# Optimization experiments

Hardware: AMD Instinct MI355X
Metric: run time of the kernel (lower is better)

## Reference

```python
import jax, jax.numpy as jnp
import numpy as np

# Dims: B batch, L seq, D model dim, A attn dim, H heads, W window, FF ff hidden
B, L, D = 4, 4096, 1024
A, H, W = 64, 1, 64
FF = 2 * D
EPS = 1e-6


def setup_inputs() -> dict:
    key = jax.random.key(0)
    ks = jax.random.split(key, 12)
    s = lambda k, shape, scale: (jax.random.normal(k, shape, jnp.float32) * scale)
    return {
        "x": s(ks[0], (B, L, D), 1.0),
        "norm1_w": jnp.ones((D,), jnp.float32),
        "norm2_w": jnp.ones((D,), jnp.float32),
        "a_raw": s(ks[1], (D,), 1.0),   # diag SSM transition (pre-sigmoid)
        "b_w": s(ks[2], (D,), 0.5),     # diag input gain
        "c_w": s(ks[3], (D,), 0.5),     # diag output gain
        "Wq": s(ks[4], (D, A), D ** -0.5),
        "Wk": s(ks[5], (D, A), D ** -0.5),
        "Wv": s(ks[6], (D, A), D ** -0.5),
        "Wo": s(ks[7], (A, D), A ** -0.5),
        "Wg": s(ks[8], (D, 1), D ** -0.5),
        "gate_bias": jnp.float32(-4.0),
        "ff_w1": s(ks[9], (D, FF), D ** -0.5),
        "ff_w2": s(ks[10], (FF, D), FF ** -0.5),
    }


def rmsnorm(x, w):
    return x * jax.lax.rsqrt(jnp.mean(x * x, -1, keepdims=True) + EPS) * w


def ssm_scan(u, a):
    # h_t = a * h_{t-1} + u_t (diagonal linear recurrence), parallel assoc scan over time
    aa = jnp.broadcast_to(a, u.shape)

    def comb(c1, c2):
        a1, b1 = c1
        a2, b2 = c2
        return a1 * a2, a2 * b1 + b2

    _, h = jax.lax.associative_scan(comb, (aa, u), axis=1)
    return h


def reference(x, norm1_w, norm2_w, a_raw, b_w, c_w, Wq, Wk, Wv, Wo, Wg, gate_bias, ff_w1, ff_w2):
    normed = rmsnorm(x, norm1_w)                      # input_norm
    a = jax.nn.sigmoid(a_raw)                         # decay in (0,1)
    h = ssm_scan(normed * b_w, a)                     # ChaosSSMCore diag scan
    x_ssm = x + h * c_w                               # residual

    # Causal sliding-window attention sidecar (window W, includes self)
    K = x_ssm @ Wk                                    # [B,L,A]
    V = x_ssm @ Wv
    hd = A // H
    q = (x_ssm @ Wq).reshape(B, L, H, hd)
    idx = jnp.arange(L)[:, None] + jnp.arange(W)[None, :] - (W - 1)  # [L,W]
    valid = idx >= 0
    idxc = jnp.clip(idx, 0, L - 1)
    Kg = K[:, idxc].reshape(B, L, W, H, hd)           # gathered window keys
    Vg = V[:, idxc].reshape(B, L, W, H, hd)
    scores = jnp.einsum('blhd,blwhd->blhw', q, Kg) / jnp.sqrt(jnp.float32(hd))
    scores = jnp.where(valid[None, :, None, :], scores, -jnp.inf)
    p = jax.nn.softmax(scores, axis=-1)
    attn = jnp.einsum('blhw,blwhd->blhd', p, Vg).reshape(B, L, A) @ Wo

    gate = jax.nn.sigmoid(x_ssm @ Wg + gate_bias)     # near-zero gate at init
    x_ssm = x_ssm + gate * attn

    n2 = rmsnorm(x_ssm, norm2_w)                      # ff_norm
    y = x_ssm + jax.nn.silu(n2 @ ff_w1) @ ff_w2       # FeedForward residual
    return y
```

## Files before the change

kernel.cpp:

```cpp
#include <hip/hip_runtime.h>
#include <math.h>

#define B_ 4
#define L_ 4096
#define D_ 1024
#define A_ 64
#define FF_ 2048
#define N_ (B_*L_)
#define EPS_ 1e-6f
#define CHUNK_ 128
#define NCHUNK_ (L_/CHUNK_)

typedef __attribute__((ext_vector_type(8))) short bf16x8;
typedef __attribute__((ext_vector_type(4))) short s16x4;
typedef __attribute__((ext_vector_type(4))) float f32x4;

static __device__ __forceinline__ float sigmoidf_(float x) { return 1.f/(1.f+expf(-x)); }
static __device__ __forceinline__ float siluf_(float x)    { return x/(1.f+expf(-x)); }

static __device__ __forceinline__ unsigned short f2bf(float f) {
    unsigned u = __float_as_uint(f);
    u += 0x7fffu + ((u >> 16) & 1u);
    return (unsigned short)(u >> 16);
}

static __device__ __forceinline__ void gload16(const short* g, short* l) {
    __builtin_amdgcn_global_load_lds(
        (const __attribute__((address_space(1))) void*)g,
        (__attribute__((address_space(3))) void*)l, 16, 0, 0);
}

__global__ __launch_bounds__(256) void rms_kernel(const float* __restrict__ x,
                                                  float* __restrict__ rms)
{
    int row  = blockIdx.x*4 + (threadIdx.x>>6);
    int lane = threadIdx.x & 63;
    const float4* xr = (const float4*)(x + (size_t)row*D_);
    float s = 0.f;
#pragma unroll
    for (int j = 0; j < 4; j++) {
        float4 v = xr[lane + 64*j];
        s += v.x*v.x + v.y*v.y + v.z*v.z + v.w*v.w;
    }
#pragma unroll
    for (int off = 32; off > 0; off >>= 1) s += __shfl_xor(s, off);
    if (lane == 0) rms[row] = rsqrtf(s*(1.f/(float)D_) + EPS_);
}

__global__ __launch_bounds__(64) void scan1_kernel(
    const float* __restrict__ x, const float* __restrict__ rms1,
    const float* __restrict__ n1w, const float* __restrict__ bw,
    const float* __restrict__ araw, float* __restrict__ cpart)
{
    int d = blockIdx.x*64 + threadIdx.x;
    int c = blockIdx.y;
    int b = blockIdx.z;
    float a = sigmoidf_(araw[d]);
    float w = n1w[d]*bw[d];
    float h = 0.f;
    size_t base = ((size_t)b*L_ + (size_t)c*CHUNK_)*D_ + d;
    const float* rp = rms1 + b*L_ + c*CHUNK_;
#pragma unroll 8
    for (int t = 0; t < CHUNK_; t++) {
        float u = x[base + (size_t)t*D_] * rp[t] * w;
        h = a*h + u;
    }
    cpart[((size_t)b*NCHUNK_ + c)*D_ + d] = h;
}

__global__ __launch_bounds__(256) void scan2_kernel(
    const float* __restrict__ araw, const float* __restrict__ cpart,
    float* __restrict__ cin)
{
    int idx = blockIdx.x*256 + threadIdx.x;
    int b = idx >> 10;
    int d = idx & (D_-1);
    float a = sigmoidf_(araw[d]);
    float aT = a;
#pragma unroll
    for (int i = 0; i < 7; i++) aT *= aT;
    float cy = 0.f;
    for (int c = 0; c < NCHUNK_; c++) {
        size_t o = ((size_t)b*NCHUNK_ + c)*D_ + d;
        cin[o] = cy;
        cy = aT*cy + cpart[o];
    }
}

__global__ __launch_bounds__(64) void scan3_kernel(
    const float* __restrict__ x, const float* __restrict__ rms1,
    const float* __restrict__ n1w, const float* __restrict__ bw,
    const float* __restrict__ cw, const float* __restrict__ araw,
    const float* __restrict__ cin, float* __restrict__ x_ssm,
    short* __restrict__ xsb)
{
    int d = blockIdx.x*64 + threadIdx.x;
    int c = blockIdx.y;
    int b = blockIdx.z;
    float a = sigmoidf_(araw[d]);
    float w = n1w[d]*bw[d];
    float cwd = cw[d];
    float h = cin[((size_t)b*NCHUNK_ + c)*D_ + d];
    size_t base = ((size_t)b*L_ + (size_t)c*CHUNK_)*D_ + d;
    const float* rp = rms1 + b*L_ + c*CHUNK_;
#pragma unroll 8
    for (int t = 0; t < CHUNK_; t++) {
        size_t p = base + (size_t)t*D_;
        float xv = x[p];
        h = a*h + xv * rp[t] * w;
        float o = xv + h*cwd;
        x_ssm[p] = o;
        xsb[p] = (short)f2bf(o);
    }
}

__global__ __launch_bounds__(256) void gate_kernel(
    const float* __restrict__ xs, const float* __restrict__ Wg,
    const float* __restrict__ gb, float* __restrict__ gate)
{
    int row  = blockIdx.x*4 + (threadIdx.x>>6);
    int lane = threadIdx.x & 63;
    const float4* xr = (const float4*)(xs + (size_t)row*D_);
    const float4* wr = (const float4*)Wg;
    float s = 0.f;
#pragma unroll
    for (int j = 0; j < 4; j++) {
        float4 xv = xr[lane + 64*j];
        float4 wv = wr[lane + 64*j];
        s += xv.x*wv.x + xv.y*wv.y + xv.z*wv.z + xv.w*wv.w;
    }
#pragma unroll
    for (int off = 32; off > 0; off >>= 1) s += __shfl_xor(s, off);
    if (lane == 0) gate[row] = sigmoidf_(s + gb[0]);
}

__global__ __launch_bounds__(256) void attn_kernel(
    const float* __restrict__ qm, const float* __restrict__ km,
    const float* __restrict__ vm, short* __restrict__ om)
{
    __shared__ float KV[128][68];
    int b  = blockIdx.y;
    int l0 = blockIdx.x*64;
    int t  = threadIdx.x;
    int r  = t >> 2;
    int qq = t & 3;

#pragma unroll
    for (int i = 0; i < 8; i++) {
        int lin = i*256 + t;
        int row = lin >> 4;
        int f4  = lin & 15;
        int gl  = l0 - 64 + row;
        float4 val = make_float4(0.f,0.f,0.f,0.f);
        if (gl >= 0) val = *(const float4*)(km + ((size_t)b*L_ + gl)*A_ + f4*4);
        *(float4*)&KV[row][f4*4] = val;
    }
    float4 qreg[16];
    {
        const float* qrow = qm + ((size_t)b*L_ + l0 + r)*A_;
#pragma unroll
        for (int j = 0; j < 16; j++) qreg[j] = *(const float4*)(qrow + j*4);
    }
    __syncthreads();

    float s[16];
#pragma unroll
    for (int wi = 0; wi < 16; wi++) {
        int w  = qq*16 + wi;
        int tr = r + w + 1;
        float dot = 0.f;
#pragma unroll
        for (int j = 0; j < 16; j++) {
            float4 kv = *(const float4*)&KV[tr][j*4];
            dot += qreg[j].x*kv.x + qreg[j].y*kv.y + qreg[j].z*kv.z + qreg[j].w*kv.w;
        }
        s[wi] = (l0 + r - 63 + w >= 0) ? dot*0.125f : -INFINITY;
    }
    float mx = s[0];
#pragma unroll
    for (int wi = 1; wi < 16; wi++) mx = fmaxf(mx, s[wi]);
    mx = fmaxf(mx, __shfl_xor(mx, 1));
    mx = fmaxf(mx, __shfl_xor(mx, 2));
    float sum = 0.f;
#pragma unroll
    for (int wi = 0; wi < 16; wi++) { s[wi] = expf(s[wi] - mx); sum += s[wi]; }
    sum += __shfl_xor(sum, 1);
    sum += __shfl_xor(sum, 2);
    float inv = 1.f/sum;
#pragma unroll
    for (int wi = 0; wi < 16; wi++) s[wi] *= inv;

    __syncthreads();
#pragma unroll
    for (int i = 0; i < 8; i++) {
        int lin = i*256 + t;
        int row = lin >> 4;
        int f4  = lin & 15;
        int gl  = l0 - 64 + row;
        float4 val = make_float4(0.f,0.f,0.f,0.f);
        if (gl >= 0) val = *(const float4*)(vm + ((size_t)b*L_ + gl)*A_ + f4*4);
        *(float4*)&KV[row][f4*4] = val;
    }
    __syncthreads();

    float4 acc[4];
#pragma unroll
    for (int ss = 0; ss < 4; ss++) acc[ss] = make_float4(0.f,0.f,0.f,0.f);
#pragma unroll
    for (int w = 0; w < 64; w++) {
        float pv = __shfl(s[w & 15], (t & 60) + (w >> 4));
        int tr = r + w + 1;
#pragma unroll
        for (int ss = 0; ss < 4; ss++) {
            float4 vv = *(const float4*)&KV[tr][qq*16 + ss*4];
            acc[ss].x += pv*vv.x; acc[ss].y += pv*vv.y;
            acc[ss].z += pv*vv.z; acc[ss].w += pv*vv.w;
        }
    }
    short* orow = om + ((size_t)b*L_ + l0 + r)*A_ + qq*16;
#pragma unroll
    for (int ss = 0; ss < 4; ss++) {
        s16x4 ov = { (short)f2bf(acc[ss].x), (short)f2bf(acc[ss].y),
                     (short)f2bf(acc[ss].z), (short)f2bf(acc[ss].w) };
        *(s16x4*)(orow + ss*4) = ov;
    }
}

__global__ __launch_bounds__(256) void cvt_transpose(
    const float* __restrict__ in, int R, int C, short* __restrict__ out)
{
    __shared__ short sh[64][68];
    int t  = threadIdx.x;
    int c0 = blockIdx.x * 64, r0 = blockIdx.y * 64;
    int rr = t >> 4, cc = (t & 15) * 4;
#pragma unroll
    for (int p = 0; p < 4; p++) {
        int r = p*16 + rr;
        float4 v = *(const float4*)(in + (size_t)(r0 + r)*C + c0 + cc);
        s16x4 sv = { (short)f2bf(v.x), (short)f2bf(v.y), (short)f2bf(v.z), (short)f2bf(v.w) };
        *(s16x4*)&sh[r][cc] = sv;
    }
    __syncthreads();
#pragma unroll
    for (int p = 0; p < 4; p++) {
        int c = p*16 + rr;
        s16x4 ov = { sh[cc+0][c], sh[cc+1][c], sh[cc+2][c], sh[cc+3][c] };
        *(s16x4*)(out + (size_t)(c0 + c)*R + r0 + cc) = ov;
    }
}

__global__ __launch_bounds__(256) void ff1prep(
    const float* __restrict__ xatt, const float* __restrict__ n2w,
    short* __restrict__ a1)
{
    int row  = blockIdx.x*4 + (threadIdx.x>>6);
    int lane = threadIdx.x & 63;
    const float4* xr = (const float4*)(xatt + (size_t)row*D_);
    const float4* wr = (const float4*)n2w;
    float4 v[4];
    float s = 0.f;
#pragma unroll
    for (int j = 0; j < 4; j++) {
        v[j] = xr[lane + 64*j];
        s += v[j].x*v[j].x + v[j].y*v[j].y + v[j].z*v[j].z + v[j].w*v[j].w;
    }
#pragma unroll
    for (int off = 32; off > 0; off >>= 1) s += __shfl_xor(s, off);
    float r = rsqrtf(s*(1.f/(float)D_) + EPS_);
#pragma unroll
    for (int j = 0; j < 4; j++) {
        float4 w = wr[lane + 64*j];
        s16x4 o = { (short)f2bf(v[j].x*r*w.x), (short)f2bf(v[j].y*r*w.y),
                    (short)f2bf(v[j].z*r*w.z), (short)f2bf(v[j].w*r*w.w) };
        *(s16x4*)(a1 + (size_t)row*D_ + (lane + 64*j)*4) = o;
    }
}

__global__ __launch_bounds__(256) void qkv_mfma(
    const short* __restrict__ A, const short* __restrict__ BT,
    float* __restrict__ qo, float* __restrict__ ko, float* __restrict__ vo)
{
    __shared__ short As2[2][64*32];
    __shared__ short Bs2[2][192*32];
    const int t = threadIdx.x, l = t & 63, w = t >> 6;
    const size_t m0 = (size_t)blockIdx.x*64;
    const short* Ab = A + m0*D_;

    const int ar = w*16 + (l&15);
    const int offA = ar*32 + (((l>>4) ^ ((ar>>1)&3)) & 3)*8;
    int offB[12];
#pragma unroll
    for (int j = 0; j < 12; j++) {
        int br = j*16 + (l&15);
        offB[j] = br*32 + (((l>>4) ^ ((br>>1)&3)) & 3)*8;
    }

#define QSTG(bi, k0) { \
        { int r = t>>2; int lc = (t&3) ^ ((r>>1)&3); \
          gload16(Ab + (size_t)r*D_ + (k0) + lc*8, &As2[bi][(w*64)*8]); } \
        _Pragma("unroll") \
        for (int i_ = 0; i_ < 3; i_++) { \
            int s_ = i_*256 + t; int r = s_>>2; int lc = (s_&3) ^ ((r>>1)&3); \
            gload16(BT + (size_t)r*D_ + (k0) + lc*8, &Bs2[bi][(i_*256 + w*64)*8]); } }

    f32x4 acc[12];
    f32x4 zero = {0.f,0.f,0.f,0.f};
#pragma unroll
    for (int j = 0; j < 12; j++) acc[j] = zero;

    QSTG(0, 0);
    __syncthreads();
    int cur = 0;
    for (int kt = 0; kt < 32; kt++) {
        if (kt + 1 < 32) QSTG(cur^1, (kt+1)*32);
        bf16x8 af = *(const bf16x8*)&As2[cur][offA];
#pragma unroll
        for (int j = 0; j < 12; j++) {
            bf16x8 bfv = *(const bf16x8*)&Bs2[cur][offB[j]];
            acc[j] = __builtin_amdgcn_mfma_f32_16x16x32_bf16(af, bfv, acc[j], 0, 0, 0);
        }
        __syncthreads();
        cur ^= 1;
    }
#pragma unroll
    for (int j = 0; j < 12; j++) {
        int col = j*16 + (l&15);
        int mat = col >> 6, c = col & 63;
        float* dst = (mat == 0) ? qo : (mat == 1) ? ko : vo;
#pragma unroll
        for (int v = 0; v < 4; v++) {
            size_t row = m0 + w*16 + (l>>4)*4 + v;
            dst[row*A_ + c] = acc[j][v];
        }
    }
#undef QSTG
}

__global__ __launch_bounds__(256) void gemm_wo(
    const short* __restrict__ A,
    const short* __restrict__ BT,
    const float* __restrict__ gate, const float* __restrict__ resid,
    float* __restrict__ Cout)
{
    __shared__ short As3[128*64];
    __shared__ short Bs3[128*64];
    const int t = threadIdx.x, l = t & 63, w = t >> 6;
    const int wm = w >> 1, wn = w & 1;
    const size_t m0 = (size_t)blockIdx.x*128, n0 = (size_t)blockIdx.y*128;

#pragma unroll
    for (int i = 0; i < 4; i++) {
        int s = i*256 + t;
        int r = s >> 3, lc = (s&7) ^ (r&7);
        gload16(A  + (m0 + r)*64 + lc*8, &As3[(i*256 + w*64)*8]);
        gload16(BT + (n0 + r)*64 + lc*8, &Bs3[(i*256 + w*64)*8]);
    }
    __syncthreads();

    f32x4 acc[4][4];
    f32x4 zero = {0.f,0.f,0.f,0.f};
#pragma unroll
    for (int i = 0; i < 4; i++)
#pragma unroll
        for (int j = 0; j < 4; j++) acc[i][j] = zero;

#pragma unroll
    for (int kk = 0; kk < 2; kk++) {
        bf16x8 af[4], bfv[4];
#pragma unroll
        for (int i = 0; i < 4; i++) {
            int ar = wm*64 + i*16 + (l&15);
            int pch = (kk*4 + (l>>4)) ^ (ar&7);
            af[i] = *(const bf16x8*)&As3[ar*64 + pch*8];
        }
#pragma unroll
        for (int j = 0; j < 4; j++) {
            int br = wn*64 + j*16 + (l&15);
            int pch = (kk*4 + (l>>4)) ^ (br&7);
            bfv[j] = *(const bf16x8*)&Bs3[br*64 + pch*8];
        }
#pragma unroll
        for (int i = 0; i < 4; i++)
#pragma unroll
            for (int j = 0; j < 4; j++)
                acc[i][j] = __builtin_amdgcn_mfma_f32_16x16x32_bf16(af[i], bfv[j], acc[i][j], 0, 0, 0);
    }

#pragma unroll
    for (int i = 0; i < 4; i++) {
#pragma unroll
        for (int v = 0; v < 4; v++) {
            size_t row = m0 + wm*64 + i*16 + (l>>4)*4 + v;
            float g = gate[row];
#pragma unroll
            for (int j = 0; j < 4; j++) {
                size_t col = n0 + wn*64 + j*16 + (l&15);
                Cout[row*D_ + col] = resid[row*D_ + col] + g*acc[i][j][v];
            }
        }
    }
}

template<int K, int MODE>
__global__ __launch_bounds__(512, 2) void gemm256(
    const short* __restrict__ A,
    const short* __restrict__ BT,
    void* __restrict__ Cout, int ldc)
{
    __shared__ short As[4][256*32];
    __shared__ short Bs[4][256*32];

    const int gy = gridDim.y;
    const int nwg = gridDim.x * gy;
    const int o = blockIdx.y * gridDim.x + blockIdx.x;
    const int q = nwg >> 3;
    const int swz = (o & 7)*q + (o >> 3);
    const int bx = swz / gy, by = swz % gy;

    const int t = threadIdx.x;
    const int l = t & 63;
    const int w = t >> 6;
    const int wm = w >> 2;
    const int wn = w & 3;
    const size_t m0 = (size_t)bx * 256;
    const size_t n0 = (size_t)by * 256;
    const short* Ab = A  + m0 * (size_t)K;
    const short* Bb = BT + n0 * (size_t)K;
    const int s0 = w*64 + l;

    int offA[8], offB[4];
#pragma unroll
    for (int i = 0; i < 8; i++) {
        int ar = wm*128 + i*16 + (l&15);
        offA[i] = ar*32 + (((l>>4) ^ ((ar>>1)&3)) & 3)*8;
    }
#pragma unroll
    for (int j = 0; j < 4; j++) {
        int br = wn*64 + j*16 + (l&15);
        offB[j] = br*32 + (((l>>4) ^ ((br>>1)&3)) & 3)*8;
    }

#define STAGE_A(bi, k0) { _Pragma("unroll") \
    for (int i_ = 0; i_ < 2; i_++) { \
        int s_ = i_*512 + s0; int r_ = s_>>2; int lc_ = (s_&3) ^ ((r_>>1)&3); \
        gload16(Ab + (size_t)r_*K + (k0) + lc_*8, &As[bi][(i_*512 + w*64)*8]); } }
#define STAGE_B(bi, k0) { _Pragma("unroll") \
    for (int i_ = 0; i_ < 2; i_++) { \
        int s_ = i_*512 + s0; int r_ = s_>>2; int lc_ = (s_&3) ^ ((r_>>1)&3); \
        gload16(Bb + (size_t)r_*K + (k0) + lc_*8, &Bs[bi][(i_*512 + w*64)*8]); } }

    f32x4 acc[8][4];
    f32x4 zero = {0.f,0.f,0.f,0.f};
#pragma unroll
    for (int i = 0; i < 8; i++)
#pragma unroll
        for (int j = 0; j < 4; j++) acc[i][j] = zero;

    STAGE_A(0, 0);  STAGE_B(0, 0);
    STAGE_A(1, 32); STAGE_B(1, 32);
    asm volatile("s_waitcnt vmcnt(4)" ::: "memory");
    __builtin_amdgcn_s_barrier();

    const int nk = K >> 5;
#pragma unroll 1
    for (int kt = 0; kt < nk; kt++) {
        const short* a_ = &As[kt & 3][0];
        const short* b_ = &Bs[kt & 3][0];
        const int prefetch = (kt + 2 < nk);
        const int pb = (kt + 2) & 3;
        const int pk = (kt + 2) << 5;

        bf16x8 bfv[4], af[4];
#pragma unroll
        for (int j = 0; j < 4; j++) bfv[j] = *(const bf16x8*)(b_ + offB[j]);
#pragma unroll
        for (int i = 0; i < 4; i++) af[i] = *(const bf16x8*)(a_ + offA[i]);
        if (prefetch) STAGE_A(pb, pk);
        __builtin_amdgcn_s_setprio(1);
#pragma unroll
        for (int i = 0; i < 4; i++)
#pragma unroll
            for (int j = 0; j < 4; j++)
                acc[i][j] = __builtin_amdgcn_mfma_f32_16x16x32_bf16(af[i], bfv[j], acc[i][j], 0, 0, 0);
        __builtin_amdgcn_s_setprio(0);

#pragma unroll
        for (int i = 0; i < 4; i++) af[i] = *(const bf16x8*)(a_ + offA[4+i]);
        if (prefetch) STAGE_B(pb, pk);
        __builtin_amdgcn_s_setprio(1);
#pragma unroll
        for (int i = 0; i < 4; i++)
#pragma unroll
            for (int j = 0; j < 4; j++)
                acc[4+i][j] = __builtin_amdgcn_mfma_f32_16x16x32_bf16(af[i], bfv[j], acc[4+i][j], 0, 0, 0);
        __builtin_amdgcn_s_setprio(0);

        if (prefetch) { asm volatile("s_waitcnt vmcnt(4)" ::: "memory"); }
        else          { asm volatile("s_waitcnt vmcnt(0)" ::: "memory"); }
        __builtin_amdgcn_s_barrier();
    }

#pragma unroll
    for (int i = 0; i < 8; i++) {
        size_t row_base = m0 + wm*128 + i*16 + (l >> 4)*4;
#pragma unroll
        for (int j = 0; j < 4; j++) {
            size_t col = n0 + wn*64 + j*16 + (l & 15);
#pragma unroll
            for (int v = 0; v < 4; v++) {
                size_t row = row_base + v;
                float val = acc[i][j][v];
                if (MODE == 0) {
                    ((short*)Cout)[row * ldc + col] = (short)f2bf(siluf_(val));
                } else {
                    float* p = (float*)Cout + row * ldc + col;
                    *p = val + *p;
                }
            }
        }
    }
#undef STAGE_A
#undef STAGE_B
}

extern "C" void kernel_launch(void* const* d_in, const int* in_sizes, int n_in,
                              void* d_out, int out_size, void* d_ws, size_t ws_size,
                              hipStream_t stream)
{
    const float* x    = (const float*)d_in[0];
    const float* n1w  = (const float*)d_in[1];
    const float* n2w  = (const float*)d_in[2];
    const float* araw = (const float*)d_in[3];
    const float* bw   = (const float*)d_in[4];
    const float* cw   = (const float*)d_in[5];
    const float* Wq   = (const float*)d_in[6];
    const float* Wk   = (const float*)d_in[7];
    const float* Wv   = (const float*)d_in[8];
    const float* Wo   = (const float*)d_in[9];
    const float* Wg   = (const float*)d_in[10];
    const float* gb   = (const float*)d_in[11];
    const float* ffw1 = (const float*)d_in[12];
    const float* ffw2 = (const float*)d_in[13];
    float* out = (float*)d_out;

    float* ws    = (float*)d_ws;
    float* rms1  = ws;
    float* gate  = rms1  + N_;
    float* cpart = gate  + N_;
    float* cin   = cpart + (size_t)B_*NCHUNK_*D_;
    float* qb    = cin   + (size_t)B_*NCHUNK_*D_;
    float* kb    = qb    + (size_t)N_*A_;
    float* vb    = kb    + (size_t)N_*A_;
    float* x_ssm = vb    + (size_t)N_*A_;
    short* xsb   = (short*)(x_ssm + (size_t)N_*D_);
    short* attnb = xsb   + (size_t)N_*D_;
    short* a1    = attnb + (size_t)N_*A_;
    short* act   = a1    + (size_t)N_*D_;
    short* w1t   = act   + (size_t)N_*FF_;
    short* w2t   = w1t   + (size_t)FF_*D_;
    short* wqkvT = w2t   + (size_t)D_*FF_;
    short* wot   = wqkvT + (size_t)192*D_;

    cvt_transpose<<<dim3(FF_/64, D_/64), 256, 0, stream>>>(ffw1, D_, FF_, w1t);
    cvt_transpose<<<dim3(D_/64, FF_/64), 256, 0, stream>>>(ffw2, FF_, D_, w2t);
    cvt_transpose<<<dim3(1, D_/64), 256, 0, stream>>>(Wq, D_, A_, wqkvT);
    cvt_transpose<<<dim3(1, D_/64), 256, 0, stream>>>(Wk, D_, A_, wqkvT + (size_t)A_*D_);
    cvt_transpose<<<dim3(1, D_/64), 256, 0, stream>>>(Wv, D_, A_, wqkvT + (size_t)2*A_*D_);
    cvt_transpose<<<dim3(D_/64, 1), 256, 0, stream>>>(Wo, A_, D_, wot);

    rms_kernel<<<N_/4, 256, 0, stream>>>(x, rms1);
    scan1_kernel<<<dim3(D_/64, NCHUNK_, B_), 64, 0, stream>>>(x, rms1, n1w, bw, araw, cpart);
    scan2_kernel<<<(B_*D_)/256, 256, 0, stream>>>(araw, cpart, cin);
    scan3_kernel<<<dim3(D_/64, NCHUNK_, B_), 64, 0, stream>>>(x, rms1, n1w, bw, cw, araw, cin, x_ssm, xsb);
    qkv_mfma<<<N_/64, 256, 0, stream>>>(xsb, wqkvT, qb, kb, vb);
    gate_kernel<<<N_/4, 256, 0, stream>>>(x_ssm, Wg, gb, gate);
    attn_kernel<<<dim3(L_/64, B_), 256, 0, stream>>>(qb, kb, vb, attnb);
    gemm_wo<<<dim3(N_/128, D_/128), 256, 0, stream>>>(attnb, wot, gate, x_ssm, out);
    ff1prep<<<N_/4, 256, 0, stream>>>(out, n2w, a1);
    gemm256<D_, 0><<<dim3(N_/256, FF_/256), 512, 0, stream>>>(a1, w1t, (void*)act, FF_);
    gemm256<FF_, 1><<<dim3(N_/256, D_/256), 512, 0, stream>>>(act, w2t, (void*)out, D_);
}
```

Baseline: 478.2 us.

## Fuse gate into QKV GEMM, MFMA attention, and restructure FF GEMM pipeline

Folds the gate projection into the QKV MFMA GEMM as an extra 16-column tile, and stores Q/K/V in bf16 plus a transposed V copy. Replaces the scalar fp32 sliding-window attention with an MFMA version: QK^T and PV go through matrix cores with swizzled LDS and a bf16 probability tile. The FF GEMMs move to a new 8-phase schedule with 64-wide K steps, interleaved partial-tile loads and double buffering. Together these aim to cut extra kernels, memory traffic and scalar FLOPs, at the cost of bf16 rounding of Q/K/V and attention probabilities.

```diff
diff --git a/kernel.cpp b/kernel.cpp
--- a/kernel.cpp
+++ b/kernel.cpp
@@ -114,118 +114,6 @@
     }
 }
 
-__global__ __launch_bounds__(256) void gate_kernel(
-    const float* __restrict__ xs, const float* __restrict__ Wg,
-    const float* __restrict__ gb, float* __restrict__ gate)
-{
-    int row  = blockIdx.x*4 + (threadIdx.x>>6);
-    int lane = threadIdx.x & 63;
-    const float4* xr = (const float4*)(xs + (size_t)row*D_);
-    const float4* wr = (const float4*)Wg;
-    float s = 0.f;
-#pragma unroll
-    for (int j = 0; j < 4; j++) {
-        float4 xv = xr[lane + 64*j];
-        float4 wv = wr[lane + 64*j];
-        s += xv.x*wv.x + xv.y*wv.y + xv.z*wv.z + xv.w*wv.w;
-    }
-#pragma unroll
-    for (int off = 32; off > 0; off >>= 1) s += __shfl_xor(s, off);
-    if (lane == 0) gate[row] = sigmoidf_(s + gb[0]);
-}
-
-__global__ __launch_bounds__(256) void attn_kernel(
-    const float* __restrict__ qm, const float* __restrict__ km,
-    const float* __restrict__ vm, short* __restrict__ om)
-{
-    __shared__ float KV[128][68];
-    int b  = blockIdx.y;
-    int l0 = blockIdx.x*64;
-    int t  = threadIdx.x;
-    int r  = t >> 2;
-    int qq = t & 3;
-
-#pragma unroll
-    for (int i = 0; i < 8; i++) {
-        int lin = i*256 + t;
-        int row = lin >> 4;
-        int f4  = lin & 15;
-        int gl  = l0 - 64 + row;
-        float4 val = make_float4(0.f,0.f,0.f,0.f);
-        if (gl >= 0) val = *(const float4*)(km + ((size_t)b*L_ + gl)*A_ + f4*4);
-        *(float4*)&KV[row][f4*4] = val;
-    }
-    float4 qreg[16];
-    {
-        const float* qrow = qm + ((size_t)b*L_ + l0 + r)*A_;
-#pragma unroll
-        for (int j = 0; j < 16; j++) qreg[j] = *(const float4*)(qrow + j*4);
-    }
-    __syncthreads();
-
-    float s[16];
-#pragma unroll
-    for (int wi = 0; wi < 16; wi++) {
-        int w  = qq*16 + wi;
-        int tr = r + w + 1;
-        float dot = 0.f;
-#pragma unroll
-        for (int j = 0; j < 16; j++) {
-            float4 kv = *(const float4*)&KV[tr][j*4];
-            dot += qreg[j].x*kv.x + qreg[j].y*kv.y + qreg[j].z*kv.z + qreg[j].w*kv.w;
-        }
-        s[wi] = (l0 + r - 63 + w >= 0) ? dot*0.125f : -INFINITY;
-    }
-    float mx = s[0];
-#pragma unroll
-    for (int wi = 1; wi < 16; wi++) mx = fmaxf(mx, s[wi]);
-    mx = fmaxf(mx, __shfl_xor(mx, 1));
-    mx = fmaxf(mx, __shfl_xor(mx, 2));
-    float sum = 0.f;
-#pragma unroll
-    for (int wi = 0; wi < 16; wi++) { s[wi] = expf(s[wi] - mx); sum += s[wi]; }
-    sum += __shfl_xor(sum, 1);
-    sum += __shfl_xor(sum, 2);
-    float inv = 1.f/sum;
-#pragma unroll
-    for (int wi = 0; wi < 16; wi++) s[wi] *= inv;
-
-    __syncthreads();
-#pragma unroll
-    for (int i = 0; i < 8; i++) {
-        int lin = i*256 + t;
-        int row = lin >> 4;
-        int f4  = lin & 15;
-        int gl  = l0 - 64 + row;
-        float4 val = make_float4(0.f,0.f,0.f,0.f);
-        if (gl >= 0) val = *(const float4*)(vm + ((size_t)b*L_ + gl)*A_ + f4*4);
-        *(float4*)&KV[row][f4*4] = val;
-    }
-    __syncthreads();
-
-    float4 acc[4];
-#pragma unroll
-    for (int ss = 0; ss < 4; ss++) acc[ss] = make_float4(0.f,0.f,0.f,0.f);
-#pragma unroll
-    for (int w = 0; w < 64; w++) {
-        float pv = __shfl(s[w & 15], (t & 60) + (w >> 4));
-        int tr = r + w + 1;
-#pragma unroll
-        for (int ss = 0; ss < 4; ss++) {
-            float4 vv = *(const float4*)&KV[tr][qq*16 + ss*4];
-            acc[ss].x += pv*vv.x; acc[ss].y += pv*vv.y;
-            acc[ss].z += pv*vv.z; acc[ss].w += pv*vv.w;
-        }
-    }
-    short* orow = om + ((size_t)b*L_ + l0 + r)*A_ + qq*16;
-#pragma unroll
-    for (int ss = 0; ss < 4; ss++) {
-        s16x4 ov = { (short)f2bf(acc[ss].x), (short)f2bf(acc[ss].y),
-                     (short)f2bf(acc[ss].z), (short)f2bf(acc[ss].w) };
-        *(s16x4*)(orow + ss*4) = ov;
-    }
-}
-
 __global__ __launch_bounds__(256) void cvt_transpose(
     const float* __restrict__ in, int R, int C, short* __restrict__ out)
 {
@@ -247,6 +135,41 @@
         s16x4 ov = { sh[cc+0][c], sh[cc+1][c], sh[cc+2][c], sh[cc+3][c] };
         *(s16x4*)(out + (size_t)(c0 + c)*R + r0 + cc) = ov;
     }
+}
+
+__global__ __launch_bounds__(256) void qkv_t3(
+    const float* __restrict__ Wq, const float* __restrict__ Wk,
+    const float* __restrict__ Wv, short* __restrict__ outall)
+{
+    __shared__ short sh[64][68];
+    const float* in = (blockIdx.z == 0) ? Wq : (blockIdx.z == 1) ? Wk : Wv;
+    short* out = outall + (size_t)blockIdx.z * A_ * D_;
+    int t  = threadIdx.x;
+    int r0 = blockIdx.y * 64;
+    int rr = t >> 4, cc = (t & 15) * 4;
+#pragma unroll
+    for (int p = 0; p < 4; p++) {
+        int r = p*16 + rr;
+        float4 v = *(const float4*)(in + (size_t)(r0 + r)*A_ + cc);
+        s16x4 sv = { (short)f2bf(v.x), (short)f2bf(v.y), (short)f2bf(v.z), (short)f2bf(v.w) };
+        *(s16x4*)&sh[r][cc] = sv;
+    }
+    __syncthreads();
+#pragma unroll
+    for (int p = 0; p < 4; p++) {
+        int c = p*16 + rr;
+        s16x4 ov = { sh[cc+0][c], sh[cc+1][c], sh[cc+2][c], sh[cc+3][c] };
+        *(s16x4*)(out + (size_t)c*D_ + r0 + cc) = ov;
+    }
+}
+
+__global__ __launch_bounds__(256) void wg_prep(const float* __restrict__ Wg,
+                                               short* __restrict__ wqkvT)
+{
+    int d = blockIdx.x*256 + threadIdx.x;
+    wqkvT[(size_t)192*D_ + d] = (short)f2bf(Wg[d]);
+#pragma unroll
+    for (int r = 193; r < 208; r++) wqkvT[(size_t)r*D_ + d] = 0;
 }
 
 __global__ __launch_bounds__(256) void ff1prep(
@@ -278,20 +201,23 @@
 
 __global__ __launch_bounds__(256) void qkv_mfma(
     const short* __restrict__ A, const short* __restrict__ BT,
-    float* __restrict__ qo, float* __restrict__ ko, float* __restrict__ vo)
+    short* __restrict__ qo, short* __restrict__ ko, short* __restrict__ vo,
+    short* __restrict__ vbt, float* __restrict__ gate,
+    const float* __restrict__ gb)
 {
     __shared__ short As2[2][64*32];
-    __shared__ short Bs2[2][192*32];
+    __shared__ short Bs2[2][208*32];
     const int t = threadIdx.x, l = t & 63, w = t >> 6;
+    const int l15 = l & 15;
     const size_t m0 = (size_t)blockIdx.x*64;
     const short* Ab = A + m0*D_;
 
-    const int ar = w*16 + (l&15);
+    const int ar = w*16 + l15;
     const int offA = ar*32 + (((l>>4) ^ ((ar>>1)&3)) & 3)*8;
-    int offB[12];
-#pragma unroll
-    for (int j = 0; j < 12; j++) {
-        int br = j*16 + (l&15);
+    int offB[13];
+#pragma unroll
+    for (int j = 0; j < 13; j++) {
+        int br = j*16 + l15;
         offB[j] = br*32 + (((l>>4) ^ ((br>>1)&3)) & 3)*8;
     }
 
@@ -301,12 +227,14 @@
         _Pragma("unroll") \
         for (int i_ = 0; i_ < 3; i_++) { \
             int s_ = i_*256 + t; int r = s_>>2; int lc = (s_&3) ^ ((r>>1)&3); \
-            gload16(BT + (size_t)r*D_ + (k0) + lc*8, &Bs2[bi][(i_*256 + w*64)*8]); } }
-
-    f32x4 acc[12];
+            gload16(BT + (size_t)r*D_ + (k0) + lc*8, &Bs2[bi][(i_*256 + w*64)*8]); } \
+        if (w == 0) { int r = 192 + (l>>2); int lc = (l&3) ^ ((r>>1)&3); \
+            gload16(BT + (size_t)r*D_ + (k0) + lc*8, &Bs2[bi][768*8]); } }
+
+    f32x4 acc[13];
     f32x4 zero = {0.f,0.f,0.f,0.f};
 #pragma unroll
-    for (int j = 0; j < 12; j++) acc[j] = zero;
+    for (int j = 0; j < 13; j++) acc[j] = zero;
 
     QSTG(0, 0);
     __syncthreads();
@@ -315,7 +243,7 @@
         if (kt + 1 < 32) QSTG(cur^1, (kt+1)*32);
         bf16x8 af = *(const bf16x8*)&As2[cur][offA];
 #pragma unroll
-        for (int j = 0; j < 12; j++) {
+        for (int j = 0; j < 13; j++) {
             bf16x8 bfv = *(const bf16x8*)&Bs2[cur][offB[j]];
             acc[j] = __builtin_amdgcn_mfma_f32_16x16x32_bf16(af, bfv, acc[j], 0, 0, 0);
         }
@@ -324,21 +252,151 @@
     }
 #pragma unroll
     for (int j = 0; j < 12; j++) {
-        int col = j*16 + (l&15);
+        int col = j*16 + l15;
         int mat = col >> 6, c = col & 63;
-        float* dst = (mat == 0) ? qo : (mat == 1) ? ko : vo;
+        short* dst = (mat == 0) ? qo : (mat == 1) ? ko : vo;
 #pragma unroll
         for (int v = 0; v < 4; v++) {
             size_t row = m0 + w*16 + (l>>4)*4 + v;
-            dst[row*A_ + c] = acc[j][v];
+            dst[row*A_ + c] = (short)f2bf(acc[j][v]);
+        }
+    }
+#pragma unroll
+    for (int j = 8; j < 12; j++) {
+        int c = j*16 + l15 - 128;
+#pragma unroll
+        for (int v = 0; v < 4; v++) {
+            size_t row = m0 + w*16 + (l>>4)*4 + v;
+            size_t bb = row >> 12;
+            size_t lr = row & (L_-1);
+            vbt[(bb*A_ + c)*L_ + lr] = (short)f2bf(acc[j][v]);
+        }
+    }
+    if (l15 == 0) {
+        float g0 = gb[0];
+#pragma unroll
+        for (int v = 0; v < 4; v++) {
+            size_t row = m0 + w*16 + (l>>4)*4 + v;
+            gate[row] = sigmoidf_(acc[12][v] + g0);
         }
     }
 #undef QSTG
 }
 
+__global__ __launch_bounds__(256) void attn_mfma(
+    const short* __restrict__ qb, const short* __restrict__ kb,
+    const short* __restrict__ vbt, short* __restrict__ om)
+{
+    __shared__ short Ks[128*64];
+    __shared__ short Vs[64*128];
+    __shared__ short Ps[64*128];
+    const int b  = blockIdx.y;
+    const int l0 = blockIdx.x*64;
+    const int t  = threadIdx.x, l = t & 63, w = t >> 6;
+    const int l15 = l & 15;
+
+#pragma unroll
+    for (int u = 0; u < 4; u++) {
+        int seg = w*4 + u;
+        int row = seg*8 + (l>>3);
+        int unit = (l&7) ^ (row&7);
+        int key = l0 - 64 + row; if (key < 0) key = 0;
+        gload16(kb + ((size_t)b*L_ + key)*A_ + unit*8, Ks + seg*512);
+    }
+#pragma unroll
+    for (int u = 0; u < 4; u++) {
+        int seg = w*4 + u;
+        int row = seg*4 + (l>>4);
+        int unit = l15 ^ (row&7);
+        int key = l0 - 64 + unit*8; if (key < 0) key = 0;
+        gload16(vbt + ((size_t)b*A_ + row)*L_ + key, Vs + seg*512);
+    }
+    bf16x8 qf[2];
+    {
+        const short* qrow = qb + ((size_t)b*L_ + l0 + w*16 + l15)*A_ + (l>>4)*8;
+        qf[0] = *(const bf16x8*)(qrow);
+        qf[1] = *(const bf16x8*)(qrow + 32);
+    }
+    asm volatile("s_waitcnt vmcnt(0)" ::: "memory");
+    __builtin_amdgcn_s_barrier();
+
+    f32x4 sacc[8];
+    f32x4 zero = {0.f,0.f,0.f,0.f};
+#pragma unroll
+    for (int j = 0; j < 8; j++) sacc[j] = zero;
+#pragma unroll
+    for (int j = 0; j < 8; j++) {
+#pragma unroll
+        for (int ks = 0; ks < 2; ks++) {
+            int row = j*16 + l15;
+            bf16x8 kf = *(const bf16x8*)(Ks + ((row*128 + ((ks*64 + (l>>4)*16) ^ ((row&7)*16))) >> 1));
+            sacc[j] = __builtin_amdgcn_mfma_f32_16x16x32_bf16(qf[ks], kf, sacc[j], 0, 0, 0);
+        }
+    }
+
+#pragma unroll
+    for (int v = 0; v < 4; v++) {
+        int gq = l0 + w*16 + (l>>4)*4 + v;
+        float m = -1e30f;
+#pragma unroll
+        for (int j = 0; j < 8; j++) {
+            int gk = l0 - 64 + j*16 + l15;
+            bool ok = (gk >= 0) && (gk <= gq) && (gk >= gq - 63);
+            float sv = ok ? sacc[j][v]*0.125f : -1e30f;
+            sacc[j][v] = sv;
+            m = fmaxf(m, sv);
+        }
+        m = fmaxf(m, __shfl_xor(m, 1));
+        m = fmaxf(m, __shfl_xor(m, 2));
+        m = fmaxf(m, __shfl_xor(m, 4));
+        m = fmaxf(m, __shfl_xor(m, 8));
+        float s = 0.f;
+#pragma unroll
+        for (int j = 0; j < 8; j++) { float e = expf(sacc[j][v] - m); sacc[j][v] = e; s += e; }
+        s += __shfl_xor(s, 1); s += __shfl_xor(s, 2);
+        s += __shfl_xor(s, 4); s += __shfl_xor(s, 8);
+        float inv = 1.f/s;
+#pragma unroll
+        for (int j = 0; j < 8; j++) sacc[j][v] *= inv;
+    }
+
+#pragma unroll
+    for (int j = 0; j < 8; j++) {
+#pragma unroll
+        for (int v = 0; v < 4; v++) {
+            int qr = w*16 + (l>>4)*4 + v;
+            int key = j*16 + l15;
+            Ps[qr*128 + (((key>>3) ^ (qr&7))*8 + (key&7))] = (short)f2bf(sacc[j][v]);
+        }
+    }
+    asm volatile("s_waitcnt lgkmcnt(0)" ::: "memory");
+
+    f32x4 oacc[4];
+#pragma unroll
+    for (int dt = 0; dt < 4; dt++) oacc[dt] = zero;
+#pragma unroll
+    for (int ks = 0; ks < 4; ks++) {
+        int qr = w*16 + l15;
+        bf16x8 pf = *(const bf16x8*)(Ps + qr*128 + (((ks*4 + (l>>4)) ^ (qr&7))*8));
+#pragma unroll
+        for (int dt = 0; dt < 4; dt++) {
+            int vr = dt*16 + l15;
+            bf16x8 vf = *(const bf16x8*)(Vs + vr*128 + (((ks*4 + (l>>4)) ^ (vr&7))*8));
+            oacc[dt] = __builtin_amdgcn_mfma_f32_16x16x32_bf16(pf, vf, oacc[dt], 0, 0, 0);
+        }
+    }
+#pragma unroll
+    for (int dt = 0; dt < 4; dt++) {
+#pragma unroll
+        for (int v = 0; v < 4; v++) {
+            int gq = l0 + w*16 + (l>>4)*4 + v;
+            om[((size_t)b*L_ + gq)*A_ + dt*16 + l15] = (short)f2bf(oacc[dt][v]);
+        }
+    }
+}
+
 __global__ __launch_bounds__(256) void gemm_wo(
-    const short* __restrict__ A,
-    const short* __restrict__ BT,
+    const short* __restrict__ A, const short* __restrict__ BT,
     const float* __restrict__ gate, const float* __restrict__ resid,
     float* __restrict__ Cout)
 {
@@ -402,52 +460,90 @@
 }
 
 template<int K, int MODE>
-__global__ __launch_bounds__(512, 2) void gemm256(
-    const short* __restrict__ A,
-    const short* __restrict__ BT,
+__global__ __launch_bounds__(512, 2) void gemm8p(
+    const short* __restrict__ A, const short* __restrict__ BT,
     void* __restrict__ Cout, int ldc)
 {
-    __shared__ short As[4][256*32];
-    __shared__ short Bs[4][256*32];
-
-    const int gy = gridDim.y;
-    const int nwg = gridDim.x * gy;
-    const int o = blockIdx.y * gridDim.x + blockIdx.x;
+    __shared__ short LDSb[65536];
+
+    const int gx = gridDim.x, gy = gridDim.y;
+    const int nwg = gx*gy;
+    const int o = blockIdx.y*gx + blockIdx.x;
     const int q = nwg >> 3;
     const int swz = (o & 7)*q + (o >> 3);
     const int bx = swz / gy, by = swz % gy;
 
-    const int t = threadIdx.x;
-    const int l = t & 63;
-    const int w = t >> 6;
-    const int wm = w >> 2;
-    const int wn = w & 3;
-    const size_t m0 = (size_t)bx * 256;
-    const size_t n0 = (size_t)by * 256;
-    const short* Ab = A  + m0 * (size_t)K;
-    const short* Bb = BT + n0 * (size_t)K;
-    const int s0 = w*64 + l;
-
-    int offA[8], offB[4];
-#pragma unroll
-    for (int i = 0; i < 8; i++) {
-        int ar = wm*128 + i*16 + (l&15);
-        offA[i] = ar*32 + (((l>>4) ^ ((ar>>1)&3)) & 3)*8;
-    }
-#pragma unroll
-    for (int j = 0; j < 4; j++) {
-        int br = wn*64 + j*16 + (l&15);
-        offB[j] = br*32 + (((l>>4) ^ ((br>>1)&3)) & 3)*8;
-    }
-
-#define STAGE_A(bi, k0) { _Pragma("unroll") \
-    for (int i_ = 0; i_ < 2; i_++) { \
-        int s_ = i_*512 + s0; int r_ = s_>>2; int lc_ = (s_&3) ^ ((r_>>1)&3); \
-        gload16(Ab + (size_t)r_*K + (k0) + lc_*8, &As[bi][(i_*512 + w*64)*8]); } }
-#define STAGE_B(bi, k0) { _Pragma("unroll") \
-    for (int i_ = 0; i_ < 2; i_++) { \
-        int s_ = i_*512 + s0; int r_ = s_>>2; int lc_ = (s_&3) ^ ((r_>>1)&3); \
-        gload16(Bb + (size_t)r_*K + (k0) + lc_*8, &Bs[bi][(i_*512 + w*64)*8]); } }
+    const int t = threadIdx.x, l = t & 63, w = t >> 6;
+    const int wm = w & 1, wn = w >> 1;
+    const size_t m0 = (size_t)bx*256, n0 = (size_t)by*256;
+
+    const int l15 = l & 15;
+    const int l16 = (l >> 4) * 16;
+    const int xsw = (l15 & 7) * 16;
+    const short* pA0 = LDSb + (((wm*16 + l15)*128 + (l16 ^ xsw)) >> 1);
+    const short* pA1 = LDSb + (((wm*16 + l15)*128 + ((64 + l16) ^ xsw)) >> 1);
+    const short* pB0 = LDSb + 32768 + (((wn*16 + l15)*128 + (l16 ^ xsw)) >> 1);
+    const short* pB1 = LDSb + 32768 + (((wn*16 + l15)*128 + ((64 + l16) ^ xsw)) >> 1);
+
+    const int srow = l >> 3;
+    const int scol = ((l & 7) ^ srow) * 8;
+    const short* gA = A  + m0*(size_t)K + (size_t)(w*8 + srow)*K + scol;
+    const short* gB = BT + n0*(size_t)K + (size_t)(w*8 + srow)*K + scol;
+    short* ldsA = (short*)LDSb + w*512;
+    short* ldsB = (short*)LDSb + 32768 + w*512;
+
+#define STG_A(DB,H,TO) { \
+    gload16(gA + (H)*128*K + (TO)*64,        ldsA + (DB)*16384 + (H)*8192); \
+    gload16(gA + (H)*128*K + 64*K + (TO)*64, ldsA + (DB)*16384 + (H)*8192 + 4096); }
+#define STG_B(DB,H,TO) { \
+    gload16(gB + (H)*128*K + (TO)*64,        ldsB + (DB)*16384 + (H)*8192); \
+    gload16(gB + (H)*128*K + 64*K + (TO)*64, ldsB + (DB)*16384 + (H)*8192 + 4096); }
+#define RD_A(DB,H,IP,KK) (*(const bf16x8*)(((KK) ? pA1 : pA0) + (DB)*16384 + (H)*8192 + (IP)*2048))
+#define RD_B(DB,H,JR,KK) (*(const bf16x8*)(((KK) ? pB1 : pB0) + (DB)*16384 + (H)*8192 + (JR)*4096))
+#define MFMA16(IO,JO) \
+    _Pragma("unroll") for (int i2 = 0; i2 < 4; i2++) \
+    _Pragma("unroll") for (int jj = 0; jj < 2; jj++) \
+    _Pragma("unroll") for (int kk = 0; kk < 2; kk++) \
+        acc[(IO)+i2][(JO)+jj] = __builtin_amdgcn_mfma_f32_16x16x32_bf16( \
+            ar[i2][kk], br[(JO)+jj][kk], acc[(IO)+i2][(JO)+jj], 0, 0, 0);
+#define PH_SYNC \
+    __builtin_amdgcn_s_barrier(); \
+    asm volatile("s_waitcnt lgkmcnt(0)" ::: "memory"); \
+    __builtin_amdgcn_sched_barrier(0);
+
+#define TILE(DB,S1,S2) { \
+     \
+    _Pragma("unroll") for (int i2 = 0; i2 < 4; i2++) { \
+        ar[i2][0] = RD_A(DB,0,i2,0); ar[i2][1] = RD_A(DB,0,i2,1); } \
+    _Pragma("unroll") for (int jj = 0; jj < 2; jj++) { \
+        br[jj][0] = RD_B(DB,0,jj,0); br[jj][1] = RD_B(DB,0,jj,1); } \
+    if (S1) { STG_A(1-(DB),1,1); \
+              asm volatile("s_waitcnt vmcnt(6)" ::: "memory"); } \
+    else    { asm volatile("s_waitcnt vmcnt(0)" ::: "memory"); } \
+    PH_SYNC \
+    __builtin_amdgcn_s_setprio(1); MFMA16(0,0) __builtin_amdgcn_s_setprio(0); \
+    __builtin_amdgcn_s_barrier(); \
+     \
+    _Pragma("unroll") for (int jj = 0; jj < 2; jj++) { \
+        br[2+jj][0] = RD_B(DB,1,jj,0); br[2+jj][1] = RD_B(DB,1,jj,1); } \
+    if (S1) STG_B(1-(DB),1,1); \
+    PH_SYNC \
+    __builtin_amdgcn_s_setprio(1); MFMA16(0,2) __builtin_amdgcn_s_setprio(0); \
+    __builtin_amdgcn_s_barrier(); \
+     \
+    _Pragma("unroll") for (int i2 = 0; i2 < 4; i2++) { \
+        ar[i2][0] = RD_A(DB,1,i2,0); ar[i2][1] = RD_A(DB,1,i2,1); } \
+    if (S2) STG_A(DB,0,2); \
+    PH_SYNC \
+    __builtin_amdgcn_s_setprio(1); MFMA16(4,0) __builtin_amdgcn_s_setprio(0); \
+    __builtin_amdgcn_s_barrier(); \
+     \
+    if (S2) STG_B(DB,0,2); \
+    __builtin_amdgcn_s_barrier(); \
+    __builtin_amdgcn_sched_barrier(0); \
+    __builtin_amdgcn_s_setprio(1); MFMA16(4,2) __builtin_amdgcn_s_setprio(0); \
+    __builtin_amdgcn_s_barrier(); \
+    gA += 64; gB += 64; }
 
     f32x4 acc[8][4];
     f32x4 zero = {0.f,0.f,0.f,0.f};
@@ -455,57 +551,29 @@
     for (int i = 0; i < 8; i++)
 #pragma unroll
         for (int j = 0; j < 4; j++) acc[i][j] = zero;
-
-    STAGE_A(0, 0);  STAGE_B(0, 0);
-    STAGE_A(1, 32); STAGE_B(1, 32);
-    asm volatile("s_waitcnt vmcnt(4)" ::: "memory");
+    bf16x8 ar[4][2], br[4][2];
+
+    STG_A(0,0,0); STG_B(0,0,0);
+    STG_A(0,1,0); STG_B(0,1,0);
+    STG_A(1,0,1); STG_B(1,0,1);
+    asm volatile("s_waitcnt vmcnt(8)" ::: "memory");
     __builtin_amdgcn_s_barrier();
 
-    const int nk = K >> 5;
+    const int nk = K >> 6;
 #pragma unroll 1
-    for (int kt = 0; kt < nk; kt++) {
-        const short* a_ = &As[kt & 3][0];
-        const short* b_ = &Bs[kt & 3][0];
-        const int prefetch = (kt + 2 < nk);
-        const int pb = (kt + 2) & 3;
-        const int pk = (kt + 2) << 5;
-
-        bf16x8 bfv[4], af[4];
-#pragma unroll
-        for (int j = 0; j < 4; j++) bfv[j] = *(const bf16x8*)(b_ + offB[j]);
-#pragma unroll
-        for (int i = 0; i < 4; i++) af[i] = *(const bf16x8*)(a_ + offA[i]);
-        if (prefetch) STAGE_A(pb, pk);
-        __builtin_amdgcn_s_setprio(1);
-#pragma unroll
-        for (int i = 0; i < 4; i++)
-#pragma unroll
-            for (int j = 0; j < 4; j++)
-                acc[i][j] = __builtin_amdgcn_mfma_f32_16x16x32_bf16(af[i], bfv[j], acc[i][j], 0, 0, 0);
-        __builtin_amdgcn_s_setprio(0);
-
-#pragma unroll
-        for (int i = 0; i < 4; i++) af[i] = *(const bf16x8*)(a_ + offA[4+i]);
-        if (prefetch) STAGE_B(pb, pk);
-        __builtin_amdgcn_s_setprio(1);
-#pragma unroll
-        for (int i = 0; i < 4; i++)
-#pragma unroll
-            for (int j = 0; j < 4; j++)
-                acc[4+i][j] = __builtin_amdgcn_mfma_f32_16x16x32_bf16(af[i], bfv[j], acc[4+i][j], 0, 0, 0);
-        __builtin_amdgcn_s_setprio(0);
-
-        if (prefetch) { asm volatile("s_waitcnt vmcnt(4)" ::: "memory"); }
-        else          { asm volatile("s_waitcnt vmcnt(0)" ::: "memory"); }
-        __builtin_amdgcn_s_barrier();
-    }
+    for (int kt2 = 0; kt2 < nk/2 - 1; kt2++) {
+        TILE(0,1,1)
+        TILE(1,1,1)
+    }
+    TILE(0,1,0)
+    TILE(1,0,0)
 
 #pragma unroll
     for (int i = 0; i < 8; i++) {
-        size_t row_base = m0 + wm*128 + i*16 + (l >> 4)*4;
+        size_t row_base = m0 + (size_t)(i>>2)*128 + (i&3)*32 + wm*16 + (l>>4)*4;
 #pragma unroll
         for (int j = 0; j < 4; j++) {
-            size_t col = n0 + wn*64 + j*16 + (l & 15);
+            size_t col = n0 + (size_t)j*64 + wn*16 + l15;
 #pragma unroll
             for (int v = 0; v < 4; v++) {
                 size_t row = row_base + v;
@@ -519,8 +587,13 @@
             }
         }
     }
-#undef STAGE_A
-#undef STAGE_B
+#undef STG_A
+#undef STG_B
+#undef RD_A
+#undef RD_B
+#undef MFMA16
+#undef PH_SYNC
+#undef TILE
 }
 
 extern "C" void kernel_launch(void* const* d_in, const int* in_sizes, int n_in,
@@ -548,35 +621,34 @@
     float* gate  = rms1  + N_;
     float* cpart = gate  + N_;
     float* cin   = cpart + (size_t)B_*NCHUNK_*D_;
-    float* qb    = cin   + (size_t)B_*NCHUNK_*D_;
-    float* kb    = qb    + (size_t)N_*A_;
-    float* vb    = kb    + (size_t)N_*A_;
-    float* x_ssm = vb    + (size_t)N_*A_;
+    float* x_ssm = cin   + (size_t)B_*NCHUNK_*D_;
     short* xsb   = (short*)(x_ssm + (size_t)N_*D_);
-    short* attnb = xsb   + (size_t)N_*D_;
+    short* qb    = xsb   + (size_t)N_*D_;
+    short* kb    = qb    + (size_t)N_*A_;
+    short* vb    = kb    + (size_t)N_*A_;
+    short* vbt   = vb    + (size_t)N_*A_;
+    short* attnb = vbt   + (size_t)N_*A_;
     short* a1    = attnb + (size_t)N_*A_;
     short* act   = a1    + (size_t)N_*D_;
     short* w1t   = act   + (size_t)N_*FF_;
     short* w2t   = w1t   + (size_t)FF_*D_;
     short* wqkvT = w2t   + (size_t)D_*FF_;
-    short* wot   = wqkvT + (size_t)192*D_;
+    short* wot   = wqkvT + (size_t)208*D_;
 
     cvt_transpose<<<dim3(FF_/64, D_/64), 256, 0, stream>>>(ffw1, D_, FF_, w1t);
     cvt_transpose<<<dim3(D_/64, FF_/64), 256, 0, stream>>>(ffw2, FF_, D_, w2t);
-    cvt_transpose<<<dim3(1, D_/64), 256, 0, stream>>>(Wq, D_, A_, wqkvT);
-    cvt_transpose<<<dim3(1, D_/64), 256, 0, stream>>>(Wk, D_, A_, wqkvT + (size_t)A_*D_);
-    cvt_transpose<<<dim3(1, D_/64), 256, 0, stream>>>(Wv, D_, A_, wqkvT + (size_t)2*A_*D_);
+    qkv_t3<<<dim3(1, D_/64, 3), 256, 0, stream>>>(Wq, Wk, Wv, wqkvT);
+    wg_prep<<<D_/256, 256, 0, stream>>>(Wg, wqkvT);
     cvt_transpose<<<dim3(D_/64, 1), 256, 0, stream>>>(Wo, A_, D_, wot);
 
     rms_kernel<<<N_/4, 256, 0, stream>>>(x, rms1);
     scan1_kernel<<<dim3(D_/64, NCHUNK_, B_), 64, 0, stream>>>(x, rms1, n1w, bw, araw, cpart);
     scan2_kernel<<<(B_*D_)/256, 256, 0, stream>>>(araw, cpart, cin);
     scan3_kernel<<<dim3(D_/64, NCHUNK_, B_), 64, 0, stream>>>(x, rms1, n1w, bw, cw, araw, cin, x_ssm, xsb);
-    qkv_mfma<<<N_/64, 256, 0, stream>>>(xsb, wqkvT, qb, kb, vb);
-    gate_kernel<<<N_/4, 256, 0, stream>>>(x_ssm, Wg, gb, gate);
-    attn_kernel<<<dim3(L_/64, B_), 256, 0, stream>>>(qb, kb, vb, attnb);
+    qkv_mfma<<<N_/64, 256, 0, stream>>>(xsb, wqkvT, qb, kb, vb, vbt, gate, gb);
+    attn_mfma<<<dim3(L_/64, B_), 256, 0, stream>>>(qb, kb, vbt, attnb);
     gemm_wo<<<dim3(N_/128, D_/128), 256, 0, stream>>>(attnb, wot, gate, x_ssm, out);
     ff1prep<<<N_/4, 256, 0, stream>>>(out, n2w, a1);
-    gemm256<D_, 0><<<dim3(N_/256, FF_/256), 512, 0, stream>>>(a1, w1t, (void*)act, FF_);
-    gemm256<FF_, 1><<<dim3(N_/256, D_/256), 512, 0, stream>>>(act, w2t, (void*)out, D_);
-}
+    gemm8p<D_, 0><<<dim3(N_/256, FF_/256), 512, 0, stream>>>(a1, w1t, (void*)act, FF_);
+    gemm8p<FF_, 1><<<dim3(N_/256, D_/256), 512, 0, stream>>>(act, w2t, (void*)out, D_);
+}
```

Measured after the change: 456.6 us. 1.05x faster.
